# Performance work log

Measured on AMD Instinct MI355X. Metric: run time of the kernel, lower is better.

## Reference

```python
import jax, jax.numpy as jnp
import numpy as np

D_MODEL = 1024
HEAD_DIM = 64
SPARSITY_RATIO = 0.1
NEG_INF = -1e9


def setup_inputs() -> dict:
    key = jax.random.key(0)
    kx, kw = jax.random.split(key)
    x = jax.random.normal(kx, (4, 4096, D_MODEL), dtype=jnp.float32)
    # nn.Linear(d_model, 3*head_dim, bias=False): weight [3*head_dim, d_model]
    W_qkv = jax.random.normal(kw, (3 * HEAD_DIM, D_MODEL), dtype=jnp.float32) / np.sqrt(D_MODEL)
    return {"x": x, "W_qkv": W_qkv}


def reference(x, W_qkv):
    B, S, _ = x.shape
    scale = HEAD_DIM ** (-0.5)
    qkv = jnp.einsum("bsd,ed->bse", x, W_qkv)  # [B,S,3*head_dim]
    q, k, v = jnp.split(qkv, 3, axis=-1)       # each [B,S,head_dim]
    scores = jnp.einsum("bqd,bkd->bqk", q, k) * scale  # [B,S,S]
    k_sparse = max(1, int(S * SPARSITY_RATIO))
    _, top_idx = jax.lax.top_k(scores, k_sparse)  # [B,S,k_sparse]
    bi = jnp.arange(B)[:, None, None]
    si = jnp.arange(S)[None, :, None]
    sparse_mask = jnp.zeros_like(scores).at[bi, si, top_idx].set(1.0)
    # attn*mask then masked_fill(mask==0, -1e9) == where(mask>0, attn, -1e9)
    masked = jnp.where(sparse_mask == 0, NEG_INF, scores * sparse_mask)
    probs = jax.nn.softmax(masked, axis=-1)
    return jnp.einsum("bqk,bkd->bqd", probs, v)
```

## Files before the change

### kernel.cpp

```cpp
#include <hip/hip_runtime.h>
#include <math.h>

#define BATCH 4
#define SEQ 4096
#define DMODEL 1024
#define HD 64
#define EE 192
#define KSP 409
#define SCALE 0.125f
#define LISTCAP 512
#define INV2048 (1.0f/2048.0f)

using half8 = __attribute__((ext_vector_type(8))) _Float16;
using half4 = __attribute__((ext_vector_type(4))) _Float16;
using f32x4 = __attribute__((ext_vector_type(4))) float;

__device__ __forceinline__ unsigned int fkey(float f) {
    unsigned int u = __float_as_uint(f);
    return (u & 0x80000000u) ? ~u : (u | 0x80000000u);
}
__device__ __forceinline__ float ikey(unsigned int k) {
    unsigned int u = (k & 0x80000000u) ? (k ^ 0x80000000u) : ~k;
    return __uint_as_float(u);
}

__global__ __launch_bounds__(256) void wsplit_kernel(const float* __restrict__ W,
                                                     _Float16* __restrict__ Whi,
                                                     _Float16* __restrict__ Wlo) {
    int i = blockIdx.x * 1024 + threadIdx.x * 4;
    float4 w = *(const float4*)&W[i];
    float f[4] = {w.x, w.y, w.z, w.w};
    half4 hv, lv;
    #pragma unroll
    for (int j = 0; j < 4; ++j) {
        _Float16 h = (_Float16)f[j];
        hv[j] = h;
        lv[j] = (_Float16)((f[j] - (float)h) * 2048.0f);
    }
    *(half4*)&Whi[i] = hv;
    *(half4*)&Wlo[i] = lv;
}

#define AH_OFF 0
#define AL_OFF 4096
#define BH_OFF 8192
#define BL_OFF 14336

__global__ __launch_bounds__(256) void qkv_mfma_kernel(const float* __restrict__ X,
        const _Float16* __restrict__ Whi, const _Float16* __restrict__ Wlo,
        _Float16* __restrict__ QH, _Float16* __restrict__ QL,
        _Float16* __restrict__ KH, _Float16* __restrict__ KL,
        float* __restrict__ V) {
    __shared__ __align__(16) unsigned char lds[20480];
    const int t = threadIdx.x;
    const int lane = t & 63;
    const int wv = t >> 6;
    const int wr = wv >> 1, wc = wv & 1;
    const int L = blockIdx.x;
    const int pair = ((L >> 4) << 3) + (L & 7);
    const int ny = (L >> 3) & 1;
    const int m0 = pair * 64;
    const int n0 = ny * 96;

    const int ar = t >> 2;
    const int akc = (t & 3) * 8;
    const int aw_addr = ((ar * 64 + (t & 3) * 16) ^ ((ar & 7) << 4));
    const int br0 = t >> 2;
    const int bw0 = ((br0 * 64 + (t & 3) * 16) ^ ((br0 & 7) << 4));
    const int br1 = 64 + (t >> 2);
    const int bw1 = ((br1 * 64 + (t & 3) * 16) ^ ((br1 & 7) << 4));

    float4 xa, xb;
    uint4 pbh0, pbl0, pbh1, pbl1;

    #define LOADG(K0) { \
        const float* xp = X + (size_t)(m0 + ar) * DMODEL + (K0) + akc; \
        xa = *(const float4*)xp; xb = *(const float4*)(xp + 4); \
        size_t wo0 = (size_t)(n0 + br0) * DMODEL + (K0) + akc; \
        pbh0 = *(const uint4*)(Whi + wo0); pbl0 = *(const uint4*)(Wlo + wo0); \
        if (t < 128) { \
            size_t wo1 = (size_t)(n0 + br1) * DMODEL + (K0) + akc; \
            pbh1 = *(const uint4*)(Whi + wo1); pbl1 = *(const uint4*)(Wlo + wo1); \
        } }

    #define WRITE_LDS() { \
        float f[8] = {xa.x, xa.y, xa.z, xa.w, xb.x, xb.y, xb.z, xb.w}; \
        half8 hv, lv; \
        _Pragma("unroll") \
        for (int i2 = 0; i2 < 8; ++i2) { \
            _Float16 h = (_Float16)f[i2]; \
            hv[i2] = h; \
            lv[i2] = (_Float16)((f[i2] - (float)h) * 2048.0f); \
        } \
        *(half8*)(lds + AH_OFF + aw_addr) = hv; \
        *(half8*)(lds + AL_OFF + aw_addr) = lv; \
        *(uint4*)(lds + BH_OFF + bw0) = pbh0; \
        *(uint4*)(lds + BL_OFF + bw0) = pbl0; \
        if (t < 128) { \
            *(uint4*)(lds + BH_OFF + bw1) = pbh1; \
            *(uint4*)(lds + BL_OFF + bw1) = pbl1; \
        } }

    f32x4 hh[2][3], xx[2][3];
    #pragma unroll
    for (int mi = 0; mi < 2; ++mi)
        #pragma unroll
        for (int ni = 0; ni < 3; ++ni) {
            hh[mi][ni] = (f32x4){0.f, 0.f, 0.f, 0.f};
            xx[mi][ni] = (f32x4){0.f, 0.f, 0.f, 0.f};
        }

    LOADG(0);
    WRITE_LDS();
    __syncthreads();

    const int kb = (lane >> 4) << 4;

    for (int it = 0; it < 32; ++it) {
        if (it < 31) LOADG((it + 1) * 32);

        half8 ah[2], al[2], bh[3], bl[3];
        #pragma unroll
        for (int mi = 0; mi < 2; ++mi) {
            int ra = wr * 32 + mi * 16 + (lane & 15);
            int ad = ((ra * 64 + kb) ^ ((ra & 7) << 4));
            ah[mi] = *(const half8*)(lds + AH_OFF + ad);
            al[mi] = *(const half8*)(lds + AL_OFF + ad);
        }
        #pragma unroll
        for (int ni = 0; ni < 3; ++ni) {
            int rb = wc * 48 + ni * 16 + (lane & 15);
            int bd = ((rb * 64 + kb) ^ ((rb & 7) << 4));
            bh[ni] = *(const half8*)(lds + BH_OFF + bd);
            bl[ni] = *(const half8*)(lds + BL_OFF + bd);
        }
        #pragma unroll
        for (int mi = 0; mi < 2; ++mi)
            #pragma unroll
            for (int ni = 0; ni < 3; ++ni) {
                hh[mi][ni] = __builtin_amdgcn_mfma_f32_16x16x32_f16(ah[mi], bh[ni], hh[mi][ni], 0, 0, 0);
                xx[mi][ni] = __builtin_amdgcn_mfma_f32_16x16x32_f16(ah[mi], bl[ni], xx[mi][ni], 0, 0, 0);
                xx[mi][ni] = __builtin_amdgcn_mfma_f32_16x16x32_f16(al[mi], bh[ni], xx[mi][ni], 0, 0, 0);
            }
        __syncthreads();
        if (it < 31) { WRITE_LDS(); __syncthreads(); }
    }

    #pragma unroll
    for (int mi = 0; mi < 2; ++mi)
        #pragma unroll
        for (int ni = 0; ni < 3; ++ni) {
            int col = n0 + wc * 48 + ni * 16 + (lane & 15);
            int rowb = m0 + wr * 32 + mi * 16 + ((lane >> 4) << 2);
            #pragma unroll
            for (int j = 0; j < 4; ++j) {
                float val = hh[mi][ni][j] + xx[mi][ni][j] * INV2048;
                int row = rowb + j;
                if (col < 64) {
                    _Float16 h = (_Float16)val;
                    QH[(size_t)row * HD + col] = h;
                    QL[(size_t)row * HD + col] = (_Float16)((val - (float)h) * 2048.0f);
                } else if (col < 128) {
                    _Float16 h = (_Float16)val;
                    KH[(size_t)row * HD + (col - 64)] = h;
                    KL[(size_t)row * HD + (col - 64)] = (_Float16)((val - (float)h) * 2048.0f);
                } else {
                    V[(size_t)row * HD + (col - 128)] = val;
                }
            }
        }
}

#define SQH_OFF 0
#define SQL_OFF 16384
#define SKH_OFF 32768
#define SKL_OFF 40960

__global__ __launch_bounds__(256) void scores_mfma_kernel(
        const _Float16* __restrict__ QH, const _Float16* __restrict__ QL,
        const _Float16* __restrict__ KH, const _Float16* __restrict__ KL,
        float* __restrict__ Sc) {
    __shared__ __align__(16) unsigned char lds[49152];
    const int t = threadIdx.x;
    const int lane = t & 63;
    const int wv = t >> 6;
    const int i0 = blockIdx.y * 128;
    const int j0 = blockIdx.x * 64;

    #pragma unroll
    for (int u = 0; u < 4; ++u) {
        int ch = t + 256 * u;
        int r = ch >> 3;
        int kbyte = (ch & 7) * 16;
        int ad = (r * 128 + kbyte) ^ ((r & 7) << 4);
        *(uint4*)(lds + SQH_OFF + ad) = *(const uint4*)((const char*)QH + (size_t)(i0 + r) * 128 + kbyte);
        *(uint4*)(lds + SQL_OFF + ad) = *(const uint4*)((const char*)QL + (size_t)(i0 + r) * 128 + kbyte);
    }
    #pragma unroll
    for (int u = 0; u < 2; ++u) {
        int ch = t + 256 * u;
        int r = ch >> 3;
        int kbyte = (ch & 7) * 16;
        int ad = (r * 128 + kbyte) ^ ((r & 7) << 4);
        *(uint4*)(lds + SKH_OFF + ad) = *(const uint4*)((const char*)KH + (size_t)(j0 + r) * 128 + kbyte);
        *(uint4*)(lds + SKL_OFF + ad) = *(const uint4*)((const char*)KL + (size_t)(j0 + r) * 128 + kbyte);
    }
    __syncthreads();

    f32x4 hh[2][4], xx[2][4];
    #pragma unroll
    for (int mi = 0; mi < 2; ++mi)
        #pragma unroll
        for (int ni = 0; ni < 4; ++ni) {
            hh[mi][ni] = (f32x4){0.f, 0.f, 0.f, 0.f};
            xx[mi][ni] = (f32x4){0.f, 0.f, 0.f, 0.f};
        }

    #pragma unroll
    for (int ks = 0; ks < 2; ++ks) {
        int kbyte = ks * 64 + ((lane >> 4) << 4);
        half8 qh[2], ql[2], kh[4], kl[4];
        #pragma unroll
        for (int mi = 0; mi < 2; ++mi) {
            int r = wv * 32 + mi * 16 + (lane & 15);
            int ad = (r * 128 + kbyte) ^ ((r & 7) << 4);
            qh[mi] = *(const half8*)(lds + SQH_OFF + ad);
            ql[mi] = *(const half8*)(lds + SQL_OFF + ad);
        }
        #pragma unroll
        for (int ni = 0; ni < 4; ++ni) {
            int r = ni * 16 + (lane & 15);
            int ad = (r * 128 + kbyte) ^ ((r & 7) << 4);
            kh[ni] = *(const half8*)(lds + SKH_OFF + ad);
            kl[ni] = *(const half8*)(lds + SKL_OFF + ad);
        }
        #pragma unroll
        for (int mi = 0; mi < 2; ++mi)
            #pragma unroll
            for (int ni = 0; ni < 4; ++ni) {
                hh[mi][ni] = __builtin_amdgcn_mfma_f32_16x16x32_f16(qh[mi], kh[ni], hh[mi][ni], 0, 0, 0);
                xx[mi][ni] = __builtin_amdgcn_mfma_f32_16x16x32_f16(qh[mi], kl[ni], xx[mi][ni], 0, 0, 0);
                xx[mi][ni] = __builtin_amdgcn_mfma_f32_16x16x32_f16(ql[mi], kh[ni], xx[mi][ni], 0, 0, 0);
            }
    }

    #pragma unroll
    for (int mi = 0; mi < 2; ++mi)
        #pragma unroll
        for (int ni = 0; ni < 4; ++ni) {
            int col = j0 + ni * 16 + (lane & 15);
            int rowb = i0 + wv * 32 + mi * 16 + ((lane >> 4) << 2);
            #pragma unroll
            for (int j = 0; j < 4; ++j) {
                float s = SCALE * (hh[mi][ni][j] + xx[mi][ni][j] * INV2048);
                Sc[(size_t)(rowb + j) * SEQ + col] = s;
            }
        }
}

__global__ __launch_bounds__(256) void topk_attn_kernel(const float* __restrict__ V,
                                                        const float* __restrict__ Sc,
                                                        float* __restrict__ Out, int b) {
    __shared__ uint2 lw[LISTCAP];
    __shared__ float pvred[1024];
    __shared__ unsigned int wredA[4];
    __shared__ unsigned int wredB[4];
    __shared__ unsigned int wsumC[4];
    __shared__ float fred0[4];
    __shared__ float fred1[4];
    __shared__ unsigned int smax4[4];

    const int t = threadIdx.x;
    const int lane = t & 63;
    const int wv = t >> 6;
    const unsigned long long ltmask = (1ull << lane) - 1ull;

    const float* row = Sc + (size_t)blockIdx.x * SEQ;
    unsigned int key[16];
    float fsum = 0.0f, fss = 0.0f;
    unsigned int mk = 0;
    #pragma unroll
    for (int u = 0; u < 4; ++u) {
        float4 v4 = *(const float4*)&row[u * 1024 + t * 4];
        float f[4] = {v4.x, v4.y, v4.z, v4.w};
        #pragma unroll
        for (int c = 0; c < 4; ++c) {
            unsigned int k = fkey(f[c]);
            key[u * 4 + c] = k;
            mk = max(mk, k);
            fsum += f[c];
            fss = fmaf(f[c], f[c], fss);
        }
    }
    #pragma unroll
    for (int off = 32; off >= 1; off >>= 1) {
        fsum += __shfl_xor(fsum, off);
        fss  += __shfl_xor(fss, off);
        mk = max(mk, (unsigned int)__shfl_xor(mk, off));
    }
    if (lane == 0) { fred0[wv] = fsum; fred1[wv] = fss; smax4[wv] = mk; }
    __syncthreads();
    const float mu = (fred0[0] + fred0[1] + fred0[2] + fred0[3]) * (1.0f / 4096.0f);
    const float ms = (fred1[0] + fred1[1] + fred1[2] + fred1[3]) * (1.0f / 4096.0f);
    const float sg = sqrtf(fmaxf(ms - mu * mu, 1e-12f));
    const float invsg = 1.0f / sg;
    const float m = ikey(max(max(smax4[0], smax4[1]), max(smax4[2], smax4[3])));

    unsigned int lo = 0u, hi = 0xFFFFFFFFu;
    float T = mu + 1.2817f * sg;
    unsigned int thrk = 0;
    bool early = false;
    int par = 0;
    for (int iter = 0; iter < 40 && lo < hi; ++iter) {
        unsigned int P;
        if (iter < 6) {
            P = fkey(T);
            if (P < lo || P >= hi) P = lo + ((hi - lo) >> 1);
        } else {
            P = lo + ((hi - lo) >> 1);
        }
        unsigned int c = 0;
        #pragma unroll
        for (int su = 0; su < 16; ++su) c += (key[su] > P) ? 1u : 0u;
        #pragma unroll
        for (int off = 32; off >= 1; off >>= 1) c += __shfl_xor(c, off);
        unsigned int* buf = par ? wredB : wredA;
        if (lane == 0) buf[wv] = c;
        __syncthreads();
        c = buf[0] + buf[1] + buf[2] + buf[3];
        par ^= 1;
        if (c >= (unsigned)KSP) {
            if (c == (unsigned)KSP) { thrk = P + 1u; early = true; break; }
            lo = P + 1u;
        } else {
            hi = P;
        }
        float Tp = ikey(P);
        float z = (Tp - mu) * invsg;
        float dens = 1634.0f * __expf(-0.5f * z * z);
        float step = ((float)(int)(c - (unsigned)KSP)) / fmaxf(dens, 8.0f);
        step = fminf(fmaxf(step, -1.0f), 1.0f);
        T = Tp + step * sg;
    }
    if (!early) thrk = lo;

    unsigned long long msk[16];
    unsigned int wt = 0;
    #pragma unroll
    for (int su = 0; su < 16; ++su) {
        msk[su] = __ballot(key[su] >= thrk);
        wt += (unsigned int)__popcll(msk[su]);
    }
    if (lane == 0) wsumC[wv] = wt;
    __syncthreads();
    unsigned int wbase = 0;
    for (int w2 = 0; w2 < wv; ++w2) wbase += wsumC[w2];
    const unsigned int total = wsumC[0] + wsumC[1] + wsumC[2] + wsumC[3];
    const int cc = (int)(total < LISTCAP ? total : LISTCAP);

    unsigned int pos = wbase;
    #pragma unroll
    for (int su = 0; su < 16; ++su) {
        if (key[su] >= thrk) {
            unsigned int myoff = pos + (unsigned int)__popcll(msk[su] & ltmask);
            if (myoff < LISTCAP) {
                unsigned int j = (unsigned)((su >> 2) * 1024 + t * 4 + (su & 3));
                lw[myoff] = make_uint2(j << 6, key[su]);
            }
        }
        pos += (unsigned int)__popcll(msk[su]);
    }
    __syncthreads();

    float lsum = 0.0f;
    #pragma unroll
    for (int r = 0; r < 2; ++r) {
        int n = t + 256 * r;
        if (n < cc) {
            uint2 e = lw[n];
            float w = __expf(ikey(e.y) - m);
            lw[n].y = __float_as_uint(w);
            lsum += w;
        }
    }
    #pragma unroll
    for (int off = 32; off >= 1; off >>= 1) lsum += __shfl_xor(lsum, off);
    if (lane == 0) fred0[wv] = lsum;
    __syncthreads();
    const float Zinv = 1.0f / (fred0[0] + fred0[1] + fred0[2] + fred0[3]);

    const int q = lane & 15;
    const int g = lane >> 4;
    const float* vbase = V + (size_t)b * SEQ * HD + 4 * q;
    float a0 = 0.f, a1 = 0.f, a2 = 0.f, a3 = 0.f;
    #pragma unroll 2
    for (int n = wv * 4 + g; n < cc; n += 16) {
        uint2 e = lw[n];
        float w = __uint_as_float(e.y);
        float4 v4 = *(const float4*)(vbase + e.x);
        a0 = fmaf(w, v4.x, a0);
        a1 = fmaf(w, v4.y, a1);
        a2 = fmaf(w, v4.z, a2);
        a3 = fmaf(w, v4.w, a3);
    }
    pvred[wv * 256 + g * 64 + 4 * q + 0] = a0;
    pvred[wv * 256 + g * 64 + 4 * q + 1] = a1;
    pvred[wv * 256 + g * 64 + 4 * q + 2] = a2;
    pvred[wv * 256 + g * 64 + 4 * q + 3] = a3;
    __syncthreads();
    if (t < 64) {
        float o = 0.f;
        #pragma unroll
        for (int w2 = 0; w2 < 4; ++w2)
            #pragma unroll
            for (int g2 = 0; g2 < 4; ++g2)
                o += pvred[w2 * 256 + g2 * 64 + t];
        Out[((size_t)b * SEQ + blockIdx.x) * HD + t] = o * Zinv;
    }
}

extern "C" void kernel_launch(void* const* d_in, const int* in_sizes, int n_in,
                              void* d_out, int out_size, void* d_ws, size_t ws_size,
                              hipStream_t stream) {
    (void)in_sizes; (void)n_in; (void)out_size; (void)ws_size;
    const float* X = (const float*)d_in[0];
    const float* W = (const float*)d_in[1];
    float* Out = (float*)d_out;

    char* ws = (char*)d_ws;
    const size_t V_BYTES  = (size_t)BATCH * SEQ * HD * 4;
    const size_t SC_BYTES = (size_t)SEQ * SEQ * 4;
    const size_t WH_BYTES = (size_t)EE * DMODEL * 2;
    const size_t QH_BYTES = (size_t)BATCH * SEQ * HD * 2;

    float*    Vv  = (float*)(ws);
    float*    sc  = (float*)(ws + V_BYTES);
    _Float16* Whi = (_Float16*)(ws + V_BYTES + SC_BYTES);
    _Float16* Wlo = (_Float16*)(ws + V_BYTES + SC_BYTES + WH_BYTES);
    _Float16* QH  = (_Float16*)(ws + V_BYTES + SC_BYTES + 2 * WH_BYTES);
    _Float16* QL  = (_Float16*)(ws + V_BYTES + SC_BYTES + 2 * WH_BYTES + QH_BYTES);
    _Float16* KH  = (_Float16*)(ws + V_BYTES + SC_BYTES + 2 * WH_BYTES + 2 * QH_BYTES);
    _Float16* KL  = (_Float16*)(ws + V_BYTES + SC_BYTES + 2 * WH_BYTES + 3 * QH_BYTES);

    wsplit_kernel<<<EE, 256, 0, stream>>>(W, Whi, Wlo);
    qkv_mfma_kernel<<<512, 256, 0, stream>>>(X, Whi, Wlo, QH, QL, KH, KL, Vv);
    for (int b = 0; b < BATCH; ++b) {
        scores_mfma_kernel<<<dim3(64, 32), 256, 0, stream>>>(
            QH + (size_t)b * SEQ * HD, QL + (size_t)b * SEQ * HD,
            KH + (size_t)b * SEQ * HD, KL + (size_t)b * SEQ * HD, sc);
        topk_attn_kernel<<<SEQ, 256, 0, stream>>>(Vv, sc, Out, b);
    }
}
```

Before: 282.2 us.

## Split QKV projection GEMM along K with separate reduction kernel

After: 290.9 us. 3.1% more time.

```diff
diff --git a/kernel.cpp b/kernel.cpp
--- a/kernel.cpp
+++ b/kernel.cpp
@@ -10,6 +10,8 @@
 #define SCALE 0.125f
 #define LISTCAP 512
 #define INV2048 (1.0f/2048.0f)
+#define ROWS (BATCH*SEQ)
+#define PSTRIDE ((size_t)ROWS*EE)
 
 using half8 = __attribute__((ext_vector_type(8))) _Float16;
 using half4 = __attribute__((ext_vector_type(4))) _Float16;
@@ -48,19 +50,18 @@
 
 __global__ __launch_bounds__(256) void qkv_mfma_kernel(const float* __restrict__ X,
         const _Float16* __restrict__ Whi, const _Float16* __restrict__ Wlo,
-        _Float16* __restrict__ QH, _Float16* __restrict__ QL,
-        _Float16* __restrict__ KH, _Float16* __restrict__ KL,
-        float* __restrict__ V) {
+        float* __restrict__ Part) {
     __shared__ __align__(16) unsigned char lds[20480];
     const int t = threadIdx.x;
     const int lane = t & 63;
     const int wv = t >> 6;
     const int wr = wv >> 1, wc = wv & 1;
-    const int L = blockIdx.x;
-    const int pair = ((L >> 4) << 3) + (L & 7);
-    const int ny = (L >> 3) & 1;
-    const int m0 = pair * 64;
+    const int id = blockIdx.x;
+    const int ks = id & 3;
+    const int ny = (id >> 2) & 1;
+    const int m0 = (id >> 3) * 64;
     const int n0 = ny * 96;
+    const int kbase = ks * 256;
 
     const int ar = t >> 2;
     const int akc = (t & 3) * 8;
@@ -110,14 +111,14 @@
             xx[mi][ni] = (f32x4){0.f, 0.f, 0.f, 0.f};
         }
 
-    LOADG(0);
+    LOADG(kbase);
     WRITE_LDS();
     __syncthreads();
 
     const int kb = (lane >> 4) << 4;
 
-    for (int it = 0; it < 32; ++it) {
-        if (it < 31) LOADG((it + 1) * 32);
+    for (int it = 0; it < 8; ++it) {
+        if (it < 7) LOADG(kbase + (it + 1) * 32);
 
         half8 ah[2], al[2], bh[3], bl[3];
         #pragma unroll
@@ -143,9 +144,10 @@
                 xx[mi][ni] = __builtin_amdgcn_mfma_f32_16x16x32_f16(al[mi], bh[ni], xx[mi][ni], 0, 0, 0);
             }
         __syncthreads();
-        if (it < 31) { WRITE_LDS(); __syncthreads(); }
-    }
-
+        if (it < 7) { WRITE_LDS(); __syncthreads(); }
+    }
+
+    float* P = Part + (size_t)ks * PSTRIDE;
     #pragma unroll
     for (int mi = 0; mi < 2; ++mi)
         #pragma unroll
@@ -154,21 +156,51 @@
             int rowb = m0 + wr * 32 + mi * 16 + ((lane >> 4) << 2);
             #pragma unroll
             for (int j = 0; j < 4; ++j) {
-                float val = hh[mi][ni][j] + xx[mi][ni][j] * INV2048;
-                int row = rowb + j;
-                if (col < 64) {
-                    _Float16 h = (_Float16)val;
-                    QH[(size_t)row * HD + col] = h;
-                    QL[(size_t)row * HD + col] = (_Float16)((val - (float)h) * 2048.0f);
-                } else if (col < 128) {
-                    _Float16 h = (_Float16)val;
-                    KH[(size_t)row * HD + (col - 64)] = h;
-                    KL[(size_t)row * HD + (col - 64)] = (_Float16)((val - (float)h) * 2048.0f);
-                } else {
-                    V[(size_t)row * HD + (col - 128)] = val;
-                }
+                P[(size_t)(rowb + j) * EE + col] = hh[mi][ni][j] + xx[mi][ni][j] * INV2048;
             }
         }
+}
+
+__global__ __launch_bounds__(256) void qkv_combine_kernel(const float* __restrict__ Part,
+        _Float16* __restrict__ QH, _Float16* __restrict__ QL,
+        _Float16* __restrict__ KH, _Float16* __restrict__ KL,
+        float* __restrict__ V) {
+    int idx = blockIdx.x * 256 + threadIdx.x;
+    int row = idx / 48;
+    int c4 = (idx - row * 48) * 4;
+    const float* p = Part + (size_t)row * EE + c4;
+    float4 a0 = *(const float4*)(p);
+    float4 a1 = *(const float4*)(p + PSTRIDE);
+    float4 a2 = *(const float4*)(p + 2 * PSTRIDE);
+    float4 a3 = *(const float4*)(p + 3 * PSTRIDE);
+    float s[4] = {(a0.x + a1.x) + (a2.x + a3.x),
+                  (a0.y + a1.y) + (a2.y + a3.y),
+                  (a0.z + a1.z) + (a2.z + a3.z),
+                  (a0.w + a1.w) + (a2.w + a3.w)};
+    if (c4 < 64) {
+        half4 h, l;
+        #pragma unroll
+        for (int j = 0; j < 4; ++j) {
+            _Float16 hv = (_Float16)s[j];
+            h[j] = hv;
+            l[j] = (_Float16)((s[j] - (float)hv) * 2048.0f);
+        }
+        *(half4*)&QH[(size_t)row * HD + c4] = h;
+        *(half4*)&QL[(size_t)row * HD + c4] = l;
+    } else if (c4 < 128) {
+        half4 h, l;
+        #pragma unroll
+        for (int j = 0; j < 4; ++j) {
+            _Float16 hv = (_Float16)s[j];
+            h[j] = hv;
+            l[j] = (_Float16)((s[j] - (float)hv) * 2048.0f);
+        }
+        *(half4*)&KH[(size_t)row * HD + (c4 - 64)] = h;
+        *(half4*)&KL[(size_t)row * HD + (c4 - 64)] = l;
+    } else {
+        float4 o = {s[0], s[1], s[2], s[3]};
+        *(float4*)&V[(size_t)row * HD + (c4 - 128)] = o;
+    }
 }
 
 #define SQH_OFF 0
@@ -433,8 +465,9 @@
     const size_t WH_BYTES = (size_t)EE * DMODEL * 2;
     const size_t QH_BYTES = (size_t)BATCH * SEQ * HD * 2;
 
-    float*    Vv  = (float*)(ws);
-    float*    sc  = (float*)(ws + V_BYTES);
+    float*    Vv   = (float*)(ws);
+    float*    sc   = (float*)(ws + V_BYTES);
+    float*    Part = sc;
     _Float16* Whi = (_Float16*)(ws + V_BYTES + SC_BYTES);
     _Float16* Wlo = (_Float16*)(ws + V_BYTES + SC_BYTES + WH_BYTES);
     _Float16* QH  = (_Float16*)(ws + V_BYTES + SC_BYTES + 2 * WH_BYTES);
@@ -443,7 +476,8 @@
     _Float16* KL  = (_Float16*)(ws + V_BYTES + SC_BYTES + 2 * WH_BYTES + 3 * QH_BYTES);
 
     wsplit_kernel<<<EE, 256, 0, stream>>>(W, Whi, Wlo);
-    qkv_mfma_kernel<<<512, 256, 0, stream>>>(X, Whi, Wlo, QH, QL, KH, KL, Vv);
+    qkv_mfma_kernel<<<2048, 256, 0, stream>>>(X, Whi, Wlo, Part);
+    qkv_combine_kernel<<<(ROWS * EE / 4) / 256, 256, 0, stream>>>(Part, QH, QL, KH, KL, Vv);
     for (int b = 0; b < BATCH; ++b) {
         scores_mfma_kernel<<<dim3(64, 32), 256, 0, stream>>>(
             QH + (size_t)b * SEQ * HD, QL + (size_t)b * SEQ * HD,
```

## Process each top-k row with a single wavefront to eliminate block barriers

Applied to the files above, without the earlier changes.

Result: slower. 420.9 us (+49.2%).

```diff
diff --git a/kernel.cpp b/kernel.cpp
--- a/kernel.cpp
+++ b/kernel.cpp
@@ -258,30 +258,21 @@
         }
 }
 
-__global__ __launch_bounds__(256) void topk_attn_kernel(const float* __restrict__ V,
-                                                        const float* __restrict__ Sc,
-                                                        float* __restrict__ Out, int b) {
+__global__ __launch_bounds__(64) void topk_attn_kernel(const float* __restrict__ V,
+                                                       const float* __restrict__ Sc,
+                                                       float* __restrict__ Out, int b) {
     __shared__ uint2 lw[LISTCAP];
-    __shared__ float pvred[1024];
-    __shared__ unsigned int wredA[4];
-    __shared__ unsigned int wredB[4];
-    __shared__ unsigned int wsumC[4];
-    __shared__ float fred0[4];
-    __shared__ float fred1[4];
-    __shared__ unsigned int smax4[4];
-
-    const int t = threadIdx.x;
-    const int lane = t & 63;
-    const int wv = t >> 6;
+
+    const int lane = threadIdx.x;
     const unsigned long long ltmask = (1ull << lane) - 1ull;
-
     const float* row = Sc + (size_t)blockIdx.x * SEQ;
-    unsigned int key[16];
+
+    unsigned int key[64];
     float fsum = 0.0f, fss = 0.0f;
     unsigned int mk = 0;
     #pragma unroll
-    for (int u = 0; u < 4; ++u) {
-        float4 v4 = *(const float4*)&row[u * 1024 + t * 4];
+    for (int u = 0; u < 16; ++u) {
+        float4 v4 = *(const float4*)&row[u * 256 + lane * 4];
         float f[4] = {v4.x, v4.y, v4.z, v4.w};
         #pragma unroll
         for (int c = 0; c < 4; ++c) {
@@ -298,19 +289,16 @@
         fss  += __shfl_xor(fss, off);
         mk = max(mk, (unsigned int)__shfl_xor(mk, off));
     }
-    if (lane == 0) { fred0[wv] = fsum; fred1[wv] = fss; smax4[wv] = mk; }
-    __syncthreads();
-    const float mu = (fred0[0] + fred0[1] + fred0[2] + fred0[3]) * (1.0f / 4096.0f);
-    const float ms = (fred1[0] + fred1[1] + fred1[2] + fred1[3]) * (1.0f / 4096.0f);
+    const float mu = fsum * (1.0f / 4096.0f);
+    const float ms = fss * (1.0f / 4096.0f);
     const float sg = sqrtf(fmaxf(ms - mu * mu, 1e-12f));
     const float invsg = 1.0f / sg;
-    const float m = ikey(max(max(smax4[0], smax4[1]), max(smax4[2], smax4[3])));
+    const float m = ikey(mk);
 
     unsigned int lo = 0u, hi = 0xFFFFFFFFu;
     float T = mu + 1.2817f * sg;
     unsigned int thrk = 0;
     bool early = false;
-    int par = 0;
     for (int iter = 0; iter < 40 && lo < hi; ++iter) {
         unsigned int P;
         if (iter < 6) {
@@ -321,14 +309,9 @@
         }
         unsigned int c = 0;
         #pragma unroll
-        for (int su = 0; su < 16; ++su) c += (key[su] > P) ? 1u : 0u;
+        for (int su = 0; su < 64; ++su) c += (key[su] > P) ? 1u : 0u;
         #pragma unroll
         for (int off = 32; off >= 1; off >>= 1) c += __shfl_xor(c, off);
-        unsigned int* buf = par ? wredB : wredA;
-        if (lane == 0) buf[wv] = c;
-        __syncthreads();
-        c = buf[0] + buf[1] + buf[2] + buf[3];
-        par ^= 1;
         if (c >= (unsigned)KSP) {
             if (c == (unsigned)KSP) { thrk = P + 1u; early = true; break; }
             lo = P + 1u;
@@ -344,38 +327,27 @@
     }
     if (!early) thrk = lo;
 
-    unsigned long long msk[16];
-    unsigned int wt = 0;
-    #pragma unroll
-    for (int su = 0; su < 16; ++su) {
-        msk[su] = __ballot(key[su] >= thrk);
-        wt += (unsigned int)__popcll(msk[su]);
-    }
-    if (lane == 0) wsumC[wv] = wt;
+    unsigned int pos = 0;
+    #pragma unroll
+    for (int su = 0; su < 64; ++su) {
+        bool sel = key[su] >= thrk;
+        unsigned long long mask = __ballot(sel);
+        if (sel) {
+            unsigned int off = pos + (unsigned int)__popcll(mask & ltmask);
+            if (off < LISTCAP) {
+                unsigned int j = (unsigned)((su >> 2) * 256 + lane * 4 + (su & 3));
+                lw[off] = make_uint2(j << 6, key[su]);
+            }
+        }
+        pos += (unsigned int)__popcll(mask);
+    }
+    const int cc = (int)(pos < LISTCAP ? pos : LISTCAP);
     __syncthreads();
-    unsigned int wbase = 0;
-    for (int w2 = 0; w2 < wv; ++w2) wbase += wsumC[w2];
-    const unsigned int total = wsumC[0] + wsumC[1] + wsumC[2] + wsumC[3];
-    const int cc = (int)(total < LISTCAP ? total : LISTCAP);
-
-    unsigned int pos = wbase;
-    #pragma unroll
-    for (int su = 0; su < 16; ++su) {
-        if (key[su] >= thrk) {
-            unsigned int myoff = pos + (unsigned int)__popcll(msk[su] & ltmask);
-            if (myoff < LISTCAP) {
-                unsigned int j = (unsigned)((su >> 2) * 1024 + t * 4 + (su & 3));
-                lw[myoff] = make_uint2(j << 6, key[su]);
-            }
-        }
-        pos += (unsigned int)__popcll(msk[su]);
-    }
-    __syncthreads();
 
     float lsum = 0.0f;
     #pragma unroll
-    for (int r = 0; r < 2; ++r) {
-        int n = t + 256 * r;
+    for (int r = 0; r < 8; ++r) {
+        int n = lane + 64 * r;
         if (n < cc) {
             uint2 e = lw[n];
             float w = __expf(ikey(e.y) - m);
@@ -385,38 +357,23 @@
     }
     #pragma unroll
     for (int off = 32; off >= 1; off >>= 1) lsum += __shfl_xor(lsum, off);
-    if (lane == 0) fred0[wv] = lsum;
+    const float Zinv = 1.0f / lsum;
     __syncthreads();
-    const float Zinv = 1.0f / (fred0[0] + fred0[1] + fred0[2] + fred0[3]);
-
-    const int q = lane & 15;
-    const int g = lane >> 4;
-    const float* vbase = V + (size_t)b * SEQ * HD + 4 * q;
-    float a0 = 0.f, a1 = 0.f, a2 = 0.f, a3 = 0.f;
-    #pragma unroll 2
-    for (int n = wv * 4 + g; n < cc; n += 16) {
+
+    const float* vbase = V + (size_t)b * SEQ * HD + lane;
+    float a0 = 0.f, a1 = 0.f;
+    int n = 0;
+    for (; n + 1 < cc; n += 2) {
+        uint2 e0 = lw[n];
+        uint2 e1 = lw[n + 1];
+        a0 = fmaf(__uint_as_float(e0.y), vbase[e0.x], a0);
+        a1 = fmaf(__uint_as_float(e1.y), vbase[e1.x], a1);
+    }
+    if (n < cc) {
         uint2 e = lw[n];
-        float w = __uint_as_float(e.y);
-        float4 v4 = *(const float4*)(vbase + e.x);
-        a0 = fmaf(w, v4.x, a0);
-        a1 = fmaf(w, v4.y, a1);
-        a2 = fmaf(w, v4.z, a2);
-        a3 = fmaf(w, v4.w, a3);
-    }
-    pvred[wv * 256 + g * 64 + 4 * q + 0] = a0;
-    pvred[wv * 256 + g * 64 + 4 * q + 1] = a1;
-    pvred[wv * 256 + g * 64 + 4 * q + 2] = a2;
-    pvred[wv * 256 + g * 64 + 4 * q + 3] = a3;
-    __syncthreads();
-    if (t < 64) {
-        float o = 0.f;
-        #pragma unroll
-        for (int w2 = 0; w2 < 4; ++w2)
-            #pragma unroll
-            for (int g2 = 0; g2 < 4; ++g2)
-                o += pvred[w2 * 256 + g2 * 64 + t];
-        Out[((size_t)b * SEQ + blockIdx.x) * HD + t] = o * Zinv;
-    }
+        a0 = fmaf(__uint_as_float(e.y), vbase[e.x], a0);
+    }
+    Out[((size_t)b * SEQ + blockIdx.x) * HD + lane] = (a0 + a1) * Zinv;
 }
 
 extern "C" void kernel_launch(void* const* d_in, const int* in_sizes, int n_in,
@@ -448,6 +405,6 @@
         scores_mfma_kernel<<<dim3(64, 32), 256, 0, stream>>>(
             QH + (size_t)b * SEQ * HD, QL + (size_t)b * SEQ * HD,
             KH + (size_t)b * SEQ * HD, KL + (size_t)b * SEQ * HD, sc);
-        topk_attn_kernel<<<SEQ, 256, 0, stream>>>(Vv, sc, Out, b);
-    }
-}
+        topk_attn_kernel<<<SEQ, 64, 0, stream>>>(Vv, sc, Out, b);
+    }
+}
```

## Select top-k threshold via shared-memory histogram with bisection fallback

Applied to the files above, without the earlier changes.

Measured after the change: 273.1 us (median of 3 runs). 3.2% less time.

```diff
diff --git a/kernel.cpp b/kernel.cpp
--- a/kernel.cpp
+++ b/kernel.cpp
@@ -261,19 +261,30 @@
 __global__ __launch_bounds__(256) void topk_attn_kernel(const float* __restrict__ V,
                                                         const float* __restrict__ Sc,
                                                         float* __restrict__ Out, int b) {
+    __shared__ unsigned int hist[4][256];
     __shared__ uint2 lw[LISTCAP];
     __shared__ float pvred[1024];
     __shared__ unsigned int wredA[4];
     __shared__ unsigned int wredB[4];
+    __shared__ unsigned int wsumS[4];
     __shared__ unsigned int wsumC[4];
     __shared__ float fred0[4];
     __shared__ float fred1[4];
     __shared__ unsigned int smax4[4];
+    __shared__ unsigned int swin[3];
+    __shared__ unsigned int cand[32];
+    __shared__ unsigned int scand;
 
     const int t = threadIdx.x;
     const int lane = t & 63;
     const int wv = t >> 6;
     const unsigned long long ltmask = (1ull << lane) - 1ull;
+
+    if (t == 0) { swin[0] = 0xFFFFFFFFu; scand = 0u; }
+    {
+        uint4 z = {0u, 0u, 0u, 0u};
+        ((uint4*)hist)[t] = z;
+    }
 
     const float* row = Sc + (size_t)blockIdx.x * SEQ;
     unsigned int key[16];
@@ -306,43 +317,123 @@
     const float invsg = 1.0f / sg;
     const float m = ikey(max(max(smax4[0], smax4[1]), max(smax4[2], smax4[3])));
 
-    unsigned int lo = 0u, hi = 0xFFFFFFFFu;
-    float T = mu + 1.2817f * sg;
+    const float blo = mu + 0.85f * sg;
+    const float bhi = mu + 1.75f * sg;
+    const float wdt = bhi - blo;
+    const bool degen = !(wdt > 0.0f);
+    const float sc256 = degen ? 0.0f : 256.0f / wdt;
+    const unsigned int kblo = fkey(blo);
+
+    if (!degen) {
+        #pragma unroll
+        for (int su = 0; su < 16; ++su) {
+            unsigned int k = key[su];
+            if (k >= kblo) {
+                int bin = (int)((ikey(k) - blo) * sc256);
+                bin = bin > 255 ? 255 : bin;
+                atomicAdd(&hist[wv][bin], 1u);
+            }
+        }
+    }
+    __syncthreads();
+
+    {
+        int bb = 255 - t;
+        unsigned int cb = hist[0][bb] + hist[1][bb] + hist[2][bb] + hist[3][bb];
+        unsigned int incl = cb;
+        #pragma unroll
+        for (int off = 1; off < 64; off <<= 1) {
+            unsigned int o = __shfl_up(incl, off);
+            if (lane >= off) incl += o;
+        }
+        if (lane == 63) wsumS[wv] = incl;
+        __syncthreads();
+        unsigned int wb = 0;
+        for (int w2 = 0; w2 < wv; ++w2) wb += wsumS[w2];
+        unsigned int sumGE = wb + incl;
+        unsigned int A = sumGE - cb;
+        if (A < (unsigned)KSP && sumGE >= (unsigned)KSP) {
+            swin[0] = (unsigned)bb; swin[1] = A; swin[2] = cb;
+        }
+    }
+    __syncthreads();
+
+    const unsigned int bwin = swin[0];
+    const bool hist_ok = (bwin != 0xFFFFFFFFu) && !degen;
+    if (hist_ok) {
+        #pragma unroll
+        for (int su = 0; su < 16; ++su) {
+            unsigned int k = key[su];
+            if (k >= kblo) {
+                int bin = (int)((ikey(k) - blo) * sc256);
+                bin = bin > 255 ? 255 : bin;
+                if ((unsigned)bin == bwin) {
+                    unsigned int id = atomicAdd(&scand, 1u);
+                    if (id < 32u) cand[id] = k;
+                }
+            }
+        }
+    }
+    __syncthreads();
+
     unsigned int thrk = 0;
-    bool early = false;
-    int par = 0;
-    for (int iter = 0; iter < 40 && lo < hi; ++iter) {
-        unsigned int P;
-        if (iter < 6) {
-            P = fkey(T);
-            if (P < lo || P >= hi) P = lo + ((hi - lo) >> 1);
+    const unsigned int nc = scand;
+    bool need_fb = (!hist_ok) || (nc > 32u);
+    if (!need_fb) {
+        unsigned int remain = (unsigned)KSP - swin[1];
+        if (remain > nc) {
+            need_fb = true;
         } else {
-            P = lo + ((hi - lo) >> 1);
-        }
-        unsigned int c = 0;
-        #pragma unroll
-        for (int su = 0; su < 16; ++su) c += (key[su] > P) ? 1u : 0u;
-        #pragma unroll
-        for (int off = 32; off >= 1; off >>= 1) c += __shfl_xor(c, off);
-        unsigned int* buf = par ? wredB : wredA;
-        if (lane == 0) buf[wv] = c;
-        __syncthreads();
-        c = buf[0] + buf[1] + buf[2] + buf[3];
-        par ^= 1;
-        if (c >= (unsigned)KSP) {
-            if (c == (unsigned)KSP) { thrk = P + 1u; early = true; break; }
-            lo = P + 1u;
-        } else {
-            hi = P;
-        }
-        float Tp = ikey(P);
-        float z = (Tp - mu) * invsg;
-        float dens = 1634.0f * __expf(-0.5f * z * z);
-        float step = ((float)(int)(c - (unsigned)KSP)) / fmaxf(dens, 8.0f);
-        step = fminf(fmaxf(step, -1.0f), 1.0f);
-        T = Tp + step * sg;
-    }
-    if (!early) thrk = lo;
+            for (unsigned int i = 0; i < nc; ++i) {
+                unsigned int v = cand[i];
+                unsigned int g = 0, e = 0;
+                for (unsigned int j2 = 0; j2 < nc; ++j2) {
+                    unsigned int u2 = cand[j2];
+                    g += (u2 > v) ? 1u : 0u;
+                    e += (u2 == v) ? 1u : 0u;
+                }
+                if (g < remain && remain <= g + e) thrk = v;
+            }
+        }
+    }
+    if (need_fb) {
+        unsigned int lo = 0u, hi = 0xFFFFFFFFu;
+        float T = mu + 1.2817f * sg;
+        bool early = false;
+        int par = 0;
+        for (int iter = 0; iter < 40 && lo < hi; ++iter) {
+            unsigned int P;
+            if (iter < 6) {
+                P = fkey(T);
+                if (P < lo || P >= hi) P = lo + ((hi - lo) >> 1);
+            } else {
+                P = lo + ((hi - lo) >> 1);
+            }
+            unsigned int c = 0;
+            #pragma unroll
+            for (int su = 0; su < 16; ++su) c += (key[su] > P) ? 1u : 0u;
+            #pragma unroll
+            for (int off = 32; off >= 1; off >>= 1) c += __shfl_xor(c, off);
+            unsigned int* buf = par ? wredB : wredA;
+            if (lane == 0) buf[wv] = c;
+            __syncthreads();
+            c = buf[0] + buf[1] + buf[2] + buf[3];
+            par ^= 1;
+            if (c >= (unsigned)KSP) {
+                if (c == (unsigned)KSP) { thrk = P + 1u; early = true; break; }
+                lo = P + 1u;
+            } else {
+                hi = P;
+            }
+            float Tp = ikey(P);
+            float z = (Tp - mu) * invsg;
+            float dens = 1634.0f * __expf(-0.5f * z * z);
+            float step = ((float)(int)(c - (unsigned)KSP)) / fmaxf(dens, 8.0f);
+            step = fminf(fmaxf(step, -1.0f), 1.0f);
+            T = Tp + step * sg;
+        }
+        if (!early) thrk = lo;
+    }
 
     unsigned long long msk[16];
     unsigned int wt = 0;
```
